# Kernel optimization log

Measured on AMD Instinct MI355X. Metric: run time of the kernel, lower is better.

## Reference

```python
import jax, jax.numpy as jnp
import numpy as np

N_NODES = 100000
N_EDGES = 1600000
D_FEAT = 64


def setup_inputs() -> dict:
    key = jax.random.key(0)
    k1, k2, k3 = jax.random.split(key, 3)
    h = jax.random.normal(k1, (N_NODES, D_FEAT), dtype=jnp.float32)
    src = jax.random.randint(k2, (N_EDGES,), 0, N_NODES, dtype=jnp.int32)
    dst = jax.random.randint(k3, (N_EDGES,), 0, N_NODES, dtype=jnp.int32)
    edge_index = jnp.stack([src, dst], axis=0)  # [2, E]
    return {"h": h, "edge_index": edge_index}


def reference(h, edge_index):
    # EdgePassing: message = src node features (gather along edges)
    # Max_aggregation: per-dst-node max over incoming messages (segment max)
    src, dst = edge_index[0], edge_index[1]
    msgs = h[src]  # [E, D] gathered mailbox, never densified per-node
    agg = jax.ops.segment_max(msgs, dst, num_segments=N_NODES)  # [N, D]
    # DGL leaves nodes with no incoming messages at zero; segment_max yields -inf
    return jnp.where(jnp.isneginf(agg), jnp.zeros_like(agg), agg)
```

## Files before the change

kernel.cpp:

```cpp
#include <hip/hip_runtime.h>

#define D_FEAT 64
#define NEG_INF_BITS 0xFF800000u
#define ENC_NEG_INF  0x007FFFFFu
#define NPB 128
#define BSHIFT 7
#define BM_BLOCK 512
#define MAXB 1024

__device__ __forceinline__ unsigned enc_f32(float v) {
    unsigned b = __float_as_uint(v);
    return ((int)b >= 0) ? (b ^ 0x80000000u) : ~b;
}
__device__ __forceinline__ float dec_f32(unsigned u) {
    return (u & 0x80000000u) ? __uint_as_float(u ^ 0x80000000u) : __uint_as_float(~u);
}

__global__ void count_kernel(const int* __restrict__ dst, int* __restrict__ counts,
                             int E, int Te, int B) {
    __shared__ int lh[MAXB];
    for (int i = threadIdx.x; i < B; i += blockDim.x) lh[i] = 0;
    __syncthreads();
    int t = blockIdx.x;
    int beg = t * Te;
    int end = min(E, beg + Te);
    int nE = (end > beg) ? (end - beg) : 0;
    int n4 = nE >> 2;
    const int4* d4 = (const int4*)(dst + beg);
    for (int k = threadIdx.x; k < n4; k += blockDim.x) {
        int4 d = d4[k];
        atomicAdd(&lh[d.x >> BSHIFT], 1);
        atomicAdd(&lh[d.y >> BSHIFT], 1);
        atomicAdd(&lh[d.z >> BSHIFT], 1);
        atomicAdd(&lh[d.w >> BSHIFT], 1);
    }
    for (int i = beg + (n4 << 2) + threadIdx.x; i < end; i += blockDim.x)
        atomicAdd(&lh[dst[i] >> BSHIFT], 1);
    __syncthreads();
    for (int i = threadIdx.x; i < B; i += blockDim.x) counts[t * B + i] = lh[i];
}

__global__ void colscan_kernel(int* __restrict__ counts, int* __restrict__ hist,
                               int T, int B) {
    int w = (blockIdx.x * blockDim.x + threadIdx.x) >> 6;
    int lane = threadIdx.x & 63;
    if (w >= B) return;
    int b = w;
    int R = T >> 6;
    int v[4], pre[4];
    int base_t = lane * R;
    for (int r = 0; r < R; ++r) v[r] = counts[(base_t + r) * B + b];
    int s = 0;
    for (int r = 0; r < R; ++r) { pre[r] = s; s += v[r]; }
    int incl = s;
    for (int off = 1; off < 64; off <<= 1) {
        int tup = __shfl_up(incl, off);
        if (lane >= off) incl += tup;
    }
    int excl = incl - s;
    for (int r = 0; r < R; ++r) counts[(base_t + r) * B + b] = excl + pre[r];
    int total = __shfl(incl, 63);
    if (lane == 0) hist[b] = total;
}

__global__ void scan_kernel(const int* __restrict__ hist, int* __restrict__ bucket_start,
                            int B) {
    __shared__ int lds[MAXB];
    int tid = threadIdx.x;
    int v = (tid < B) ? hist[tid] : 0;
    lds[tid] = v;
    __syncthreads();
    for (int off = 1; off < MAXB; off <<= 1) {
        int t = (tid >= off) ? lds[tid - off] : 0;
        __syncthreads();
        lds[tid] += t;
        __syncthreads();
    }
    if (tid < B) {
        bucket_start[tid] = lds[tid] - v;
        if (tid == B - 1) bucket_start[B] = lds[tid];
    }
}

__global__ void place_kernel(const int* __restrict__ src, const int* __restrict__ dst,
                             const int* __restrict__ counts, const int* __restrict__ bucket_start,
                             unsigned* __restrict__ packed, int E, int Te, int B) {
    __shared__ int lcur[MAXB];
    int t = blockIdx.x;
    for (int i = threadIdx.x; i < B; i += blockDim.x)
        lcur[i] = bucket_start[i] + counts[t * B + i];
    __syncthreads();
    int beg = t * Te;
    int end = min(E, beg + Te);
    for (int i = beg + threadIdx.x; i < end; i += blockDim.x) {
        int d = dst[i];
        int b = d >> BSHIFT;
        int pos = atomicAdd(&lcur[b], 1);
        packed[pos] = (unsigned)src[i] | ((unsigned)(d & (NPB - 1)) << 17);
    }
}

__global__ void __launch_bounds__(BM_BLOCK)
bucket_max_kernel(const float* __restrict__ h,
                  const int* __restrict__ bucket_start,
                  const unsigned* __restrict__ packed,
                  float* __restrict__ out, int N) {
    __shared__ unsigned buf[NPB * D_FEAT];
    int b = blockIdx.x;
    int tid = threadIdx.x;
    int node0 = b << BSHIFT;
    int nvals = (min(NPB, N - node0)) * D_FEAT;

    for (int i = tid; i < NPB * D_FEAT; i += BM_BLOCK) buf[i] = ENC_NEG_INF;
    __syncthreads();

    int beg = bucket_start[b];
    int end = bucket_start[b + 1];
    int wid = tid >> 6;
    int lane = tid & 63;

    for (int base = beg + (wid << 6); base < end; base += BM_BLOCK) {
        int nk = min(64, end - base);
        unsigned p = (lane < nk) ? packed[base + lane] : 0u;
        int j = 0;
        for (; j + 8 <= nk; j += 8) {
            unsigned q[8];
            float v[8];
            #pragma unroll
            for (int k = 0; k < 8; ++k) q[k] = (unsigned)__shfl((int)p, j + k);
            #pragma unroll
            for (int k = 0; k < 8; ++k) v[k] = h[(q[k] & 0x1FFFFu) * D_FEAT + lane];
            #pragma unroll
            for (int k = 0; k < 8; ++k)
                atomicMax(&buf[(q[k] >> 17) * D_FEAT + lane], enc_f32(v[k]));
        }
        for (; j < nk; ++j) {
            unsigned pj = (unsigned)__shfl((int)p, j);
            float v = h[(pj & 0x1FFFFu) * D_FEAT + lane];
            atomicMax(&buf[(pj >> 17) * D_FEAT + lane], enc_f32(v));
        }
    }
    __syncthreads();

    for (int i = tid; i < nvals; i += BM_BLOCK) {
        unsigned u = buf[i];
        out[node0 * D_FEAT + i] = (u == ENC_NEG_INF) ? 0.0f : dec_f32(u);
    }
}

__global__ void init_out_kernel(uint4* __restrict__ out, int n4) {
    int i = blockIdx.x * blockDim.x + threadIdx.x;
    if (i < n4) {
        uint4 v;
        v.x = NEG_INF_BITS; v.y = NEG_INF_BITS; v.z = NEG_INF_BITS; v.w = NEG_INF_BITS;
        out[i] = v;
    }
}
__global__ void scatter_max_kernel(const float* __restrict__ h, const int* __restrict__ src,
                                   const int* __restrict__ dst, float* __restrict__ out, int E) {
    int gid = blockIdx.x * blockDim.x + threadIdx.x;
    int e = gid >> 6;
    if (e >= E) return;
    int lane = gid & 63;
    float v = h[src[e] * D_FEAT + lane];
    int* addr = (int*)(out + dst[e] * D_FEAT + lane);
    if (v >= 0.0f) atomicMax(addr, __float_as_int(v));
    else           atomicMin((unsigned int*)addr, __float_as_uint(v));
}
__global__ void finalize_kernel(float* __restrict__ out, int n) {
    int i = blockIdx.x * blockDim.x + threadIdx.x;
    if (i < n && __float_as_uint(out[i]) == NEG_INF_BITS) out[i] = 0.0f;
}

extern "C" void kernel_launch(void* const* d_in, const int* in_sizes, int n_in,
                              void* d_out, int out_size, void* d_ws, size_t ws_size,
                              hipStream_t stream) {
    const float* h = (const float*)d_in[0];
    const int* edge_index = (const int*)d_in[1];
    int E = in_sizes[1] / 2;
    const int* src = edge_index;
    const int* dst = edge_index + E;
    float* out = (float*)d_out;
    int N = out_size / D_FEAT;

    int B = (N + NPB - 1) >> BSHIFT;

    int T = 0;
    for (int cand = 256; cand >= 64; cand >>= 1) {
        size_t need = ((size_t)cand * B + B + (B + 1) + (size_t)E) * sizeof(int);
        if (ws_size >= need) { T = cand; break; }
    }

    if (N <= (1 << 17) && B <= MAXB && T > 0) {
        int* counts       = (int*)d_ws;
        int* hist         = counts + (size_t)T * B;
        int* bucket_start = hist + B;
        unsigned* packed  = (unsigned*)(bucket_start + B + 1);

        int Te = ((E + T - 1) / T + 3) & ~3;

        count_kernel<<<T, 512, 0, stream>>>(dst, counts, E, Te, B);
        int cs_blocks = (B * 64 + 511) / 512;
        colscan_kernel<<<cs_blocks, 512, 0, stream>>>(counts, hist, T, B);
        scan_kernel<<<1, MAXB, 0, stream>>>(hist, bucket_start, B);
        place_kernel<<<T, 512, 0, stream>>>(src, dst, counts, bucket_start, packed, E, Te, B);
        bucket_max_kernel<<<B, BM_BLOCK, 0, stream>>>(h, bucket_start, packed, out, N);
    } else {
        int n4 = out_size / 4;
        init_out_kernel<<<(n4 + 255) / 256, 256, 0, stream>>>((uint4*)out, n4);
        long long total = (long long)E * 64;
        scatter_max_kernel<<<(int)((total + 255) / 256), 256, 0, stream>>>(h, src, dst, out, E);
        finalize_kernel<<<(out_size + 255) / 256, 256, 0, stream>>>(out, out_size);
    }
}
```

Before: 163.5 us.

## Halve bucket size, add persistent work-stealing bucket kernel, rework scans and placement

```diff
diff --git a/kernel.cpp b/kernel.cpp
--- a/kernel.cpp
+++ b/kernel.cpp
@@ -3,10 +3,11 @@
 #define D_FEAT 64
 #define NEG_INF_BITS 0xFF800000u
 #define ENC_NEG_INF  0x007FFFFFu
-#define NPB 128
-#define BSHIFT 7
+#define NPB 64
+#define BSHIFT 6
 #define BM_BLOCK 512
-#define MAXB 1024
+#define BM_GRID 1024
+#define MAXB 2048
 
 __device__ __forceinline__ unsigned enc_f32(float v) {
     unsigned b = __float_as_uint(v);
@@ -24,61 +25,84 @@
     int t = blockIdx.x;
     int beg = t * Te;
     int end = min(E, beg + Te);
-    int nE = (end > beg) ? (end - beg) : 0;
-    int n4 = nE >> 2;
-    const int4* d4 = (const int4*)(dst + beg);
-    for (int k = threadIdx.x; k < n4; k += blockDim.x) {
-        int4 d = d4[k];
-        atomicAdd(&lh[d.x >> BSHIFT], 1);
-        atomicAdd(&lh[d.y >> BSHIFT], 1);
-        atomicAdd(&lh[d.z >> BSHIFT], 1);
-        atomicAdd(&lh[d.w >> BSHIFT], 1);
-    }
-    for (int i = beg + (n4 << 2) + threadIdx.x; i < end; i += blockDim.x)
-        atomicAdd(&lh[dst[i] >> BSHIFT], 1);
+    if ((E & 3) == 0) {
+        int n4 = (end > beg) ? ((end - beg) >> 2) : 0;
+        const int4* d4 = (const int4*)(dst + beg);
+        for (int k = threadIdx.x; k < n4; k += blockDim.x) {
+            int4 d = d4[k];
+            atomicAdd(&lh[d.x >> BSHIFT], 1);
+            atomicAdd(&lh[d.y >> BSHIFT], 1);
+            atomicAdd(&lh[d.z >> BSHIFT], 1);
+            atomicAdd(&lh[d.w >> BSHIFT], 1);
+        }
+        for (int i = beg + (n4 << 2) + threadIdx.x; i < end; i += blockDim.x)
+            atomicAdd(&lh[dst[i] >> BSHIFT], 1);
+    } else {
+        for (int i = beg + threadIdx.x; i < end; i += blockDim.x)
+            atomicAdd(&lh[dst[i] >> BSHIFT], 1);
+    }
     __syncthreads();
     for (int i = threadIdx.x; i < B; i += blockDim.x) counts[t * B + i] = lh[i];
 }
 
 __global__ void colscan_kernel(int* __restrict__ counts, int* __restrict__ hist,
                                int T, int B) {
-    int w = (blockIdx.x * blockDim.x + threadIdx.x) >> 6;
+    __shared__ int part[8][64];
     int lane = threadIdx.x & 63;
-    if (w >= B) return;
-    int b = w;
-    int R = T >> 6;
-    int v[4], pre[4];
-    int base_t = lane * R;
-    for (int r = 0; r < R; ++r) v[r] = counts[(base_t + r) * B + b];
+    int wid = threadIdx.x >> 6;
+    int b = (blockIdx.x << 6) + lane;
+    bool ok = b < B;
+    int Tc = (T + 7) >> 3;
+    int t0 = wid * Tc;
+    int t1 = min(T, t0 + Tc);
+
     int s = 0;
-    for (int r = 0; r < R; ++r) { pre[r] = s; s += v[r]; }
-    int incl = s;
-    for (int off = 1; off < 64; off <<= 1) {
-        int tup = __shfl_up(incl, off);
-        if (lane >= off) incl += tup;
-    }
-    int excl = incl - s;
-    for (int r = 0; r < R; ++r) counts[(base_t + r) * B + b] = excl + pre[r];
-    int total = __shfl(incl, 63);
-    if (lane == 0) hist[b] = total;
+    if (ok) {
+        #pragma unroll 4
+        for (int t = t0; t < t1; ++t) s += counts[t * B + b];
+    }
+    part[wid][lane] = s;
+    __syncthreads();
+
+    int base = 0, total = 0;
+    #pragma unroll
+    for (int w = 0; w < 8; ++w) {
+        int pv = part[w][lane];
+        if (w < wid) base += pv;
+        total += pv;
+    }
+    if (ok) {
+        if (wid == 0) hist[b] = total;
+        int run = base;
+        for (int t = t0; t < t1; ++t) {
+            int v = counts[t * B + b];
+            counts[t * B + b] = run;
+            run += v;
+        }
+    }
 }
 
 __global__ void scan_kernel(const int* __restrict__ hist, int* __restrict__ bucket_start,
-                            int B) {
-    __shared__ int lds[MAXB];
+                            int* __restrict__ counter, int B) {
+    __shared__ int lds[2048];
     int tid = threadIdx.x;
-    int v = (tid < B) ? hist[tid] : 0;
-    lds[tid] = v;
-    __syncthreads();
-    for (int off = 1; off < MAXB; off <<= 1) {
-        int t = (tid >= off) ? lds[tid - off] : 0;
-        __syncthreads();
-        lds[tid] += t;
-        __syncthreads();
-    }
-    if (tid < B) {
-        bucket_start[tid] = lds[tid] - v;
-        if (tid == B - 1) bucket_start[B] = lds[tid];
+    int p0 = tid, p1 = tid + 1024;
+    lds[p0] = (p0 < B) ? hist[p0] : 0;
+    lds[p1] = (p1 < B) ? hist[p1] : 0;
+    __syncthreads();
+    for (int off = 1; off < 2048; off <<= 1) {
+        int a0 = (p0 >= off) ? lds[p0 - off] : 0;
+        int a1 = (p1 >= off) ? lds[p1 - off] : 0;
+        __syncthreads();
+        lds[p0] += a0;
+        lds[p1] += a1;
+        __syncthreads();
+    }
+    if (p0 < B) bucket_start[p0] = lds[p0] - hist[p0];
+    if (p1 < B) bucket_start[p1] = lds[p1] - hist[p1];
+    if (tid == 0) {
+        bucket_start[B] = lds[B - 1];
+        counter[0] = 0;
     }
 }
 
@@ -92,11 +116,33 @@
     __syncthreads();
     int beg = t * Te;
     int end = min(E, beg + Te);
-    for (int i = beg + threadIdx.x; i < end; i += blockDim.x) {
-        int d = dst[i];
-        int b = d >> BSHIFT;
-        int pos = atomicAdd(&lcur[b], 1);
-        packed[pos] = (unsigned)src[i] | ((unsigned)(d & (NPB - 1)) << 17);
+    if ((E & 3) == 0) {
+        int n4 = (end > beg) ? ((end - beg) >> 2) : 0;
+        const int4* d4 = (const int4*)(dst + beg);
+        const int4* s4 = (const int4*)(src + beg);
+        for (int k = threadIdx.x; k < n4; k += blockDim.x) {
+            int4 d = d4[k];
+            int4 s = s4[k];
+            int p0 = atomicAdd(&lcur[d.x >> BSHIFT], 1);
+            __builtin_nontemporal_store((unsigned)s.x | ((unsigned)(d.x & (NPB - 1)) << 17), &packed[p0]);
+            int p1 = atomicAdd(&lcur[d.y >> BSHIFT], 1);
+            __builtin_nontemporal_store((unsigned)s.y | ((unsigned)(d.y & (NPB - 1)) << 17), &packed[p1]);
+            int p2 = atomicAdd(&lcur[d.z >> BSHIFT], 1);
+            __builtin_nontemporal_store((unsigned)s.z | ((unsigned)(d.z & (NPB - 1)) << 17), &packed[p2]);
+            int p3 = atomicAdd(&lcur[d.w >> BSHIFT], 1);
+            __builtin_nontemporal_store((unsigned)s.w | ((unsigned)(d.w & (NPB - 1)) << 17), &packed[p3]);
+        }
+        for (int i = beg + (n4 << 2) + threadIdx.x; i < end; i += blockDim.x) {
+            int d = dst[i];
+            int pos = atomicAdd(&lcur[d >> BSHIFT], 1);
+            __builtin_nontemporal_store((unsigned)src[i] | ((unsigned)(d & (NPB - 1)) << 17), &packed[pos]);
+        }
+    } else {
+        for (int i = beg + threadIdx.x; i < end; i += blockDim.x) {
+            int d = dst[i];
+            int pos = atomicAdd(&lcur[d >> BSHIFT], 1);
+            __builtin_nontemporal_store((unsigned)src[i] | ((unsigned)(d & (NPB - 1)) << 17), &packed[pos]);
+        }
     }
 }
 
@@ -104,47 +150,55 @@
 bucket_max_kernel(const float* __restrict__ h,
                   const int* __restrict__ bucket_start,
                   const unsigned* __restrict__ packed,
-                  float* __restrict__ out, int N) {
+                  float* __restrict__ out, int* __restrict__ counter,
+                  int N, int B) {
     __shared__ unsigned buf[NPB * D_FEAT];
-    int b = blockIdx.x;
+    __shared__ int task_s;
     int tid = threadIdx.x;
-    int node0 = b << BSHIFT;
-    int nvals = (min(NPB, N - node0)) * D_FEAT;
-
-    for (int i = tid; i < NPB * D_FEAT; i += BM_BLOCK) buf[i] = ENC_NEG_INF;
-    __syncthreads();
-
-    int beg = bucket_start[b];
-    int end = bucket_start[b + 1];
     int wid = tid >> 6;
     int lane = tid & 63;
 
-    for (int base = beg + (wid << 6); base < end; base += BM_BLOCK) {
-        int nk = min(64, end - base);
-        unsigned p = (lane < nk) ? packed[base + lane] : 0u;
-        int j = 0;
-        for (; j + 8 <= nk; j += 8) {
-            unsigned q[8];
-            float v[8];
-            #pragma unroll
-            for (int k = 0; k < 8; ++k) q[k] = (unsigned)__shfl((int)p, j + k);
-            #pragma unroll
-            for (int k = 0; k < 8; ++k) v[k] = h[(q[k] & 0x1FFFFu) * D_FEAT + lane];
-            #pragma unroll
-            for (int k = 0; k < 8; ++k)
-                atomicMax(&buf[(q[k] >> 17) * D_FEAT + lane], enc_f32(v[k]));
-        }
-        for (; j < nk; ++j) {
-            unsigned pj = (unsigned)__shfl((int)p, j);
-            float v = h[(pj & 0x1FFFFu) * D_FEAT + lane];
-            atomicMax(&buf[(pj >> 17) * D_FEAT + lane], enc_f32(v));
-        }
-    }
-    __syncthreads();
-
-    for (int i = tid; i < nvals; i += BM_BLOCK) {
-        unsigned u = buf[i];
-        out[node0 * D_FEAT + i] = (u == ENC_NEG_INF) ? 0.0f : dec_f32(u);
+    for (;;) {
+        if (tid == 0) task_s = atomicAdd(counter, 1);
+        __syncthreads();
+        int b = task_s;
+        if (b >= B) return;
+
+        for (int i = tid; i < NPB * D_FEAT; i += BM_BLOCK) buf[i] = ENC_NEG_INF;
+        __syncthreads();
+
+        int beg = bucket_start[b];
+        int end = bucket_start[b + 1];
+
+        for (int base = beg + (wid << 6); base < end; base += BM_BLOCK) {
+            int nk = min(64, end - base);
+            unsigned p = (lane < nk) ? __builtin_nontemporal_load(&packed[base + lane]) : 0u;
+            int j = 0;
+            for (; j + 8 <= nk; j += 8) {
+                unsigned q[8];
+                float v[8];
+                #pragma unroll
+                for (int k = 0; k < 8; ++k) q[k] = (unsigned)__shfl((int)p, j + k);
+                #pragma unroll
+                for (int k = 0; k < 8; ++k) v[k] = h[(q[k] & 0x1FFFFu) * D_FEAT + lane];
+                #pragma unroll
+                for (int k = 0; k < 8; ++k)
+                    atomicMax(&buf[(q[k] >> 17) * D_FEAT + lane], enc_f32(v[k]));
+            }
+            for (; j < nk; ++j) {
+                unsigned pj = (unsigned)__shfl((int)p, j);
+                float v = h[(pj & 0x1FFFFu) * D_FEAT + lane];
+                atomicMax(&buf[(pj >> 17) * D_FEAT + lane], enc_f32(v));
+            }
+        }
+        __syncthreads();
+
+        int node0 = b << BSHIFT;
+        int nvals = (min(NPB, N - node0)) * D_FEAT;
+        for (int i = tid; i < nvals; i += BM_BLOCK) {
+            unsigned u = buf[i];
+            out[node0 * D_FEAT + i] = (u == ENC_NEG_INF) ? 0.0f : dec_f32(u);
+        }
     }
 }
 
@@ -186,8 +240,8 @@
     int B = (N + NPB - 1) >> BSHIFT;
 
     int T = 0;
-    for (int cand = 256; cand >= 64; cand >>= 1) {
-        size_t need = ((size_t)cand * B + B + (B + 1) + (size_t)E) * sizeof(int);
+    for (int cand = 512; cand >= 64; cand >>= 1) {
+        size_t need = ((size_t)cand * B + B + (B + 1) + 1 + (size_t)E) * sizeof(int);
         if (ws_size >= need) { T = cand; break; }
     }
 
@@ -195,16 +249,18 @@
         int* counts       = (int*)d_ws;
         int* hist         = counts + (size_t)T * B;
         int* bucket_start = hist + B;
-        unsigned* packed  = (unsigned*)(bucket_start + B + 1);
+        int* counter      = bucket_start + B + 1;
+        unsigned* packed  = (unsigned*)(counter + 1);
 
         int Te = ((E + T - 1) / T + 3) & ~3;
 
         count_kernel<<<T, 512, 0, stream>>>(dst, counts, E, Te, B);
-        int cs_blocks = (B * 64 + 511) / 512;
-        colscan_kernel<<<cs_blocks, 512, 0, stream>>>(counts, hist, T, B);
-        scan_kernel<<<1, MAXB, 0, stream>>>(hist, bucket_start, B);
+        colscan_kernel<<<(B + 63) / 64, 512, 0, stream>>>(counts, hist, T, B);
+        scan_kernel<<<1, 1024, 0, stream>>>(hist, bucket_start, counter, B);
         place_kernel<<<T, 512, 0, stream>>>(src, dst, counts, bucket_start, packed, E, Te, B);
-        bucket_max_kernel<<<B, BM_BLOCK, 0, stream>>>(h, bucket_start, packed, out, N);
+        int bm_grid = (B < BM_GRID) ? B : BM_GRID;
+        bucket_max_kernel<<<bm_grid, BM_BLOCK, 0, stream>>>(h, bucket_start, packed, out,
+                                                            counter, N, B);
     } else {
         int n4 = out_size / 4;
         init_out_kernel<<<(n4 + 255) / 256, 256, 0, stream>>>((uint4*)out, n4);
```

New measurement: 218.5 us. 1.34x slower.
